# Kernel optimization log

Hardware: AMD Instinct MI355X
Metric: run time of the kernel (lower is better)

The kernel has to match this reference:

```python
import jax, jax.numpy as jnp
import numpy as np

ALPHA = 0.01  # alpha = input_scale * weight_scale (dequant scale)
BETA = 1.0    # bias scale, fixed to 1.0 in forward


def setup_inputs() -> dict:
    key = jax.random.key(0)
    k1, k2, k3 = jax.random.split(key, 3)
    # int8 values carried in int32 containers (schema has no int8 dtype)
    x = jax.random.randint(k1, (2, 2048, 4096), -127, 128, dtype=jnp.int32)
    weight = jax.random.randint(k2, (11008, 4096), -127, 128, dtype=jnp.int32)
    bias = jax.random.normal(k3, (1, 11008), dtype=jnp.float32)
    return {"x": x, "weight": weight, "bias": bias}


def reference(x, weight, bias):
    # x: [..., K] int8 activations, weight: [N, K] int8, bias: [1, N] fp32
    x_shape = x.shape
    x2 = x.reshape(-1, x_shape[-1]).astype(jnp.int8)   # [M, K]
    w8 = weight.astype(jnp.int8)                        # [N, K]
    acc = jnp.einsum('mk,nk->mn', x2, w8, preferred_element_type=jnp.int32)
    # fused dequant scale + fp32 bias add
    y = ALPHA * acc.astype(jnp.float32) + BETA * bias   # [M, N]
    return y.reshape(*x_shape[:-1], -1)
```

## Files before the change

### kernel.cpp

```cpp
#include <hip/hip_runtime.h>


#define M_DIM 4096
#define N_DIM 11008
#define K_DIM 4096
#define BM 128
#define BN 128
#define BK 64
#define ALPHA 0.01f

typedef __attribute__((ext_vector_type(4))) int i32x4;

static __device__ __forceinline__ int pack4(int4 v) {
    return (v.x & 0xff) | ((v.y & 0xff) << 8) |
           ((v.z & 0xff) << 16) | ((unsigned)(v.w & 0xff) << 24);
}

__global__ __launch_bounds__(256) void pack_i8_kernel(
    const int4* __restrict__ in, int4* __restrict__ out, int n16)
{
    int i = blockIdx.x * blockDim.x + threadIdx.x;
    if (i < n16) {
        const int4* p = in + (size_t)4 * i;
        int4 a = p[0], b = p[1], c = p[2], d = p[3];
        int4 r;
        r.x = pack4(a); r.y = pack4(b); r.z = pack4(c); r.w = pack4(d);
        out[i] = r;
    }
}

__global__ __launch_bounds__(256) void gemm_i8_kernel(
    const char* __restrict__ A,
    const char* __restrict__ B,
    const float* __restrict__ bias,
    float* __restrict__ C)
{
    __shared__ __attribute__((aligned(16))) char As[BM * BK];
    __shared__ __attribute__((aligned(16))) char Bs[BN * BK];

    const int tid  = threadIdx.x;
    const int lane = tid & 63;
    const int wave = tid >> 6;
    const int waveM = (wave >> 1) * 64;
    const int waveN = (wave & 1) * 64;
    const int bm = blockIdx.y * BM;
    const int bn = blockIdx.x * BN;

    const int lrow  = lane & 15;
    const int lquad = lane >> 4;

    const int srow = tid >> 2;
    const int scol = ((tid & 3) ^ (srow & 3)) * 16;
    const char* Abase = A + (size_t)(bm + srow) * K_DIM + scol;
    const char* Bbase = B + (size_t)(bn + srow) * K_DIM + scol;

    const int swq = (lquad ^ (lrow & 3)) * 16;

    i32x4 acc[4][4] = {};

    for (int k0 = 0; k0 < K_DIM; k0 += BK) {
        __builtin_amdgcn_global_load_lds(
            (const __attribute__((address_space(1))) void*)(Abase + k0),
            (__attribute__((address_space(3))) void*)(As + tid * 16), 16, 0, 0);
        __builtin_amdgcn_global_load_lds(
            (const __attribute__((address_space(1))) void*)(Abase + (size_t)64 * K_DIM + k0),
            (__attribute__((address_space(3))) void*)(As + 4096 + tid * 16), 16, 0, 0);
        __builtin_amdgcn_global_load_lds(
            (const __attribute__((address_space(1))) void*)(Bbase + k0),
            (__attribute__((address_space(3))) void*)(Bs + tid * 16), 16, 0, 0);
        __builtin_amdgcn_global_load_lds(
            (const __attribute__((address_space(1))) void*)(Bbase + (size_t)64 * K_DIM + k0),
            (__attribute__((address_space(3))) void*)(Bs + 4096 + tid * 16), 16, 0, 0);
        __syncthreads();

        i32x4 a[4], b[4];
#pragma unroll
        for (int i = 0; i < 4; i++)
            a[i] = *(const i32x4*)(As + (waveM + i * 16 + lrow) * BK + swq);
#pragma unroll
        for (int j = 0; j < 4; j++)
            b[j] = *(const i32x4*)(Bs + (waveN + j * 16 + lrow) * BK + swq);

#pragma unroll
        for (int i = 0; i < 4; i++)
#pragma unroll
            for (int j = 0; j < 4; j++)
                acc[i][j] = __builtin_amdgcn_mfma_i32_16x16x64_i8(a[i], b[j], acc[i][j], 0, 0, 0);

        __syncthreads();
    }

#pragma unroll
    for (int i = 0; i < 4; i++) {
        const int r0 = bm + waveM + i * 16 + lquad * 4;
#pragma unroll
        for (int j = 0; j < 4; j++) {
            const int c0 = bn + waveN + j * 16 + lrow;
            const float bv = bias[c0];
#pragma unroll
            for (int r = 0; r < 4; r++) {
                C[(size_t)(r0 + r) * N_DIM + c0] = ALPHA * (float)acc[i][j][r] + bv;
            }
        }
    }
}

extern "C" void kernel_launch(void* const* d_in, const int* in_sizes, int n_in,
                              void* d_out, int out_size, void* d_ws, size_t ws_size,
                              hipStream_t stream) {
    const int*   x    = (const int*)d_in[0];
    const int*   w    = (const int*)d_in[1];
    const float* bias = (const float*)d_in[2];
    float*       out  = (float*)d_out;

    char* Ap = (char*)d_ws;
    char* Wp = (char*)d_ws + (size_t)M_DIM * K_DIM;

    const int n16x = M_DIM * K_DIM / 16;
    const int n16w = N_DIM * K_DIM / 16;
    pack_i8_kernel<<<n16x / 256, 256, 0, stream>>>((const int4*)x, (int4*)Ap, n16x);
    pack_i8_kernel<<<n16w / 256, 256, 0, stream>>>((const int4*)w, (int4*)Wp, n16w);

    dim3 grid(N_DIM / BN, M_DIM / BM);
    gemm_i8_kernel<<<grid, 256, 0, stream>>>(Ap, Wp, bias, out);
}
```

Measured before the change: 587.3 us.

## Enlarge GEMM M-tile to 256, retune LDS swizzle, merge pack kernels

Doubles the block tile in M so each wave computes a 128x64 output with 8x4 MFMA accumulators. This raises arithmetic intensity per LDS load of B and halves B global reloads. The LDS XOR swizzle is changed to match the new read pattern, to reduce bank conflicts. The two int32-to-int8 pack launches are merged into one kernel to save a launch. The larger accumulator array raises register pressure, and launch_bounds(256,2) may force spills or limit occupancy.

Result: faster. 555.5 us (-5.4%).

```diff
diff --git a/kernel.cpp b/kernel.cpp
--- a/kernel.cpp
+++ b/kernel.cpp
@@ -4,7 +4,7 @@
 #define M_DIM 4096
 #define N_DIM 11008
 #define K_DIM 4096
-#define BM 128
+#define BM 256
 #define BN 128
 #define BK 64
 #define ALPHA 0.01f
@@ -17,19 +17,24 @@
 }
 
 __global__ __launch_bounds__(256) void pack_i8_kernel(
-    const int4* __restrict__ in, int4* __restrict__ out, int n16)
+    const int4* __restrict__ x, int4* __restrict__ xout, int n16x,
+    const int4* __restrict__ w, int4* __restrict__ wout, int n16_total)
 {
     int i = blockIdx.x * blockDim.x + threadIdx.x;
-    if (i < n16) {
-        const int4* p = in + (size_t)4 * i;
-        int4 a = p[0], b = p[1], c = p[2], d = p[3];
-        int4 r;
-        r.x = pack4(a); r.y = pack4(b); r.z = pack4(c); r.w = pack4(d);
-        out[i] = r;
-    }
+    if (i >= n16_total) return;
+    const int4* src;
+    int4* dst;
+    int idx;
+    if (i < n16x) { src = x; dst = xout; idx = i; }
+    else          { src = w; dst = wout; idx = i - n16x; }
+    const int4* p = src + (size_t)4 * idx;
+    int4 a = p[0], b = p[1], c = p[2], d = p[3];
+    int4 r;
+    r.x = pack4(a); r.y = pack4(b); r.z = pack4(c); r.w = pack4(d);
+    dst[idx] = r;
 }
 
-__global__ __launch_bounds__(256) void gemm_i8_kernel(
+__global__ __launch_bounds__(256, 2) void gemm_i8_kernel(
     const char* __restrict__ A,
     const char* __restrict__ B,
     const float* __restrict__ bias,
@@ -41,7 +46,7 @@
     const int tid  = threadIdx.x;
     const int lane = tid & 63;
     const int wave = tid >> 6;
-    const int waveM = (wave >> 1) * 64;
+    const int waveM = (wave >> 1) * 128;
     const int waveN = (wave & 1) * 64;
     const int bm = blockIdx.y * BM;
     const int bn = blockIdx.x * BN;
@@ -50,39 +55,37 @@
     const int lquad = lane >> 4;
 
     const int srow = tid >> 2;
-    const int scol = ((tid & 3) ^ (srow & 3)) * 16;
+    const int scol = ((tid & 3) ^ ((tid >> 3) & 3)) * 16;
     const char* Abase = A + (size_t)(bm + srow) * K_DIM + scol;
     const char* Bbase = B + (size_t)(bn + srow) * K_DIM + scol;
 
-    const int swq = (lquad ^ (lrow & 3)) * 16;
+    const int swq = (lquad ^ ((lrow >> 1) & 3)) * 16;
 
-    i32x4 acc[4][4] = {};
+    i32x4 acc[8][4] = {};
 
     for (int k0 = 0; k0 < K_DIM; k0 += BK) {
-        __builtin_amdgcn_global_load_lds(
-            (const __attribute__((address_space(1))) void*)(Abase + k0),
-            (__attribute__((address_space(3))) void*)(As + tid * 16), 16, 0, 0);
-        __builtin_amdgcn_global_load_lds(
-            (const __attribute__((address_space(1))) void*)(Abase + (size_t)64 * K_DIM + k0),
-            (__attribute__((address_space(3))) void*)(As + 4096 + tid * 16), 16, 0, 0);
-        __builtin_amdgcn_global_load_lds(
-            (const __attribute__((address_space(1))) void*)(Bbase + k0),
-            (__attribute__((address_space(3))) void*)(Bs + tid * 16), 16, 0, 0);
-        __builtin_amdgcn_global_load_lds(
-            (const __attribute__((address_space(1))) void*)(Bbase + (size_t)64 * K_DIM + k0),
-            (__attribute__((address_space(3))) void*)(Bs + 4096 + tid * 16), 16, 0, 0);
+#pragma unroll
+        for (int c = 0; c < 4; c++)
+            __builtin_amdgcn_global_load_lds(
+                (const __attribute__((address_space(1))) void*)(Abase + (size_t)(64 * c) * K_DIM + k0),
+                (__attribute__((address_space(3))) void*)(As + c * 4096 + tid * 16), 16, 0, 0);
+#pragma unroll
+        for (int c = 0; c < 2; c++)
+            __builtin_amdgcn_global_load_lds(
+                (const __attribute__((address_space(1))) void*)(Bbase + (size_t)(64 * c) * K_DIM + k0),
+                (__attribute__((address_space(3))) void*)(Bs + c * 4096 + tid * 16), 16, 0, 0);
         __syncthreads();
 
-        i32x4 a[4], b[4];
+        i32x4 a[8], b[4];
 #pragma unroll
-        for (int i = 0; i < 4; i++)
+        for (int i = 0; i < 8; i++)
             a[i] = *(const i32x4*)(As + (waveM + i * 16 + lrow) * BK + swq);
 #pragma unroll
         for (int j = 0; j < 4; j++)
             b[j] = *(const i32x4*)(Bs + (waveN + j * 16 + lrow) * BK + swq);
 
 #pragma unroll
-        for (int i = 0; i < 4; i++)
+        for (int i = 0; i < 8; i++)
 #pragma unroll
             for (int j = 0; j < 4; j++)
                 acc[i][j] = __builtin_amdgcn_mfma_i32_16x16x64_i8(a[i], b[j], acc[i][j], 0, 0, 0);
@@ -91,7 +94,7 @@
     }
 
 #pragma unroll
-    for (int i = 0; i < 4; i++) {
+    for (int i = 0; i < 8; i++) {
         const int r0 = bm + waveM + i * 16 + lquad * 4;
 #pragma unroll
         for (int j = 0; j < 4; j++) {
@@ -118,8 +121,9 @@
 
     const int n16x = M_DIM * K_DIM / 16;
     const int n16w = N_DIM * K_DIM / 16;
-    pack_i8_kernel<<<n16x / 256, 256, 0, stream>>>((const int4*)x, (int4*)Ap, n16x);
-    pack_i8_kernel<<<n16w / 256, 256, 0, stream>>>((const int4*)w, (int4*)Wp, n16w);
+    const int n16  = n16x + n16w;
+    pack_i8_kernel<<<n16 / 256, 256, 0, stream>>>(
+        (const int4*)x, (int4*)Ap, n16x, (const int4*)w, (int4*)Wp, n16);
 
     dim3 grid(N_DIM / BN, M_DIM / BM);
     gemm_i8_kernel<<<grid, 256, 0, stream>>>(Ap, Wp, bias, out);
```
